# Performance work log

Measured on AMD Instinct MI355X. Metric: run time of the kernel, lower is better.

Reference implementation:

```python
import jax, jax.numpy as jnp
import numpy as np

NUM_HEADS = 16


def rotate_half(x):
    h = x.shape[-1] // 2
    return jnp.concatenate([-x[..., h:], x[..., :h]], axis=-1)


def setup_inputs() -> dict:
    key = jax.random.key(0)
    ks = jax.random.split(key, 8)
    S, dim, hd = 8192, 1280, 80
    n_seg = 8
    hidden_states = jax.random.normal(ks[0], (S, dim), dtype=jnp.float32)
    cu_seqlens = (jnp.arange(n_seg + 1, dtype=jnp.int32) * (S // n_seg))
    ang = jax.random.uniform(ks[1], (S, hd), dtype=jnp.float32) * (2.0 * np.pi)
    cos = jnp.cos(ang)
    sin = jnp.sin(ang)
    qkv_w = jax.random.normal(ks[2], (3 * dim, dim), dtype=jnp.float32) * (dim ** -0.5)
    qkv_b = jax.random.normal(ks[3], (3 * dim,), dtype=jnp.float32) * 0.02
    proj_w = jax.random.normal(ks[4], (dim, dim), dtype=jnp.float32) * (dim ** -0.5)
    proj_b = jax.random.normal(ks[5], (dim,), dtype=jnp.float32) * 0.02
    return {"hidden_states": hidden_states, "cu_seqlens": cu_seqlens,
            "cos": cos, "sin": sin, "qkv_w": qkv_w, "qkv_b": qkv_b,
            "proj_w": proj_w, "proj_b": proj_b}


def reference(hidden_states, cu_seqlens, cos, sin, qkv_w, qkv_b, proj_w, proj_b):
    S, dim = hidden_states.shape
    H = NUM_HEADS
    hd = dim // H
    scaling = hd ** -0.5

    # qkv projection: [S, 3*dim] -> [S, 3, H, hd]
    qkv = (hidden_states @ qkv_w.T + qkv_b).reshape(S, 3, H, hd)
    q, k, v = qkv[:, 0], qkv[:, 1], qkv[:, 2]  # each [S, H, hd]

    # RoPE in float32, cos/sin broadcast over heads
    c = cos[:, None, :].astype(jnp.float32)
    s = sin[:, None, :].astype(jnp.float32)
    qf, kf = q.astype(jnp.float32), k.astype(jnp.float32)
    q = (qf * c + rotate_half(qf) * s).astype(q.dtype)
    k = (kf * c + rotate_half(kf) * s).astype(k.dtype)

    # Block-diagonal varlen attention: equal-length segments -> batch dim
    lengths = np.diff(np.asarray(cu_seqlens))
    L = int(lengths[0])
    assert (lengths == L).all(), "reference assumes uniform segment lengths"
    B = lengths.shape[0]
    qb = q.reshape(B, L, H, hd)
    kb = k.reshape(B, L, H, hd)
    vb = v.reshape(B, L, H, hd)

    scores = jnp.einsum('blhd,bmhd->bhlm', qb, kb) * scaling
    probs = jax.nn.softmax(scores.astype(jnp.float32), axis=-1).astype(scores.dtype)
    out = jnp.einsum('bhlm,bmhd->blhd', probs, vb).reshape(S, dim)

    return out @ proj_w.T + proj_b
```

## Files before the change

### kernel.cpp

```cpp
#include <hip/hip_runtime.h>
#include <math.h>

typedef _Float16 f16;
typedef _Float16 half8 __attribute__((ext_vector_type(8)));
typedef _Float16 half4v __attribute__((ext_vector_type(4)));
typedef _Float16 half2v __attribute__((ext_vector_type(2)));
typedef float floatx4 __attribute__((ext_vector_type(4)));
typedef unsigned int u32;

#define AS1 __attribute__((address_space(1)))
#define AS3 __attribute__((address_space(3)))

__device__ __forceinline__ void stage16(f16* l, const f16* g) {
    __builtin_amdgcn_global_load_lds((const AS1 u32*)g, (AS3 u32*)l, 16, 0, 0);
}

__global__ __launch_bounds__(256) void cvt_f32_f16(const float* __restrict__ in,
                                                   f16* __restrict__ out, int n4) {
    int i = blockIdx.x * blockDim.x + threadIdx.x;
    if (i >= n4) return;
    float4 v = ((const float4*)in)[i];
    half4v h = {(f16)v.x, (f16)v.y, (f16)v.z, (f16)v.w};
    ((half4v*)out)[i] = h;
}

constexpr int GK = 1280;

__global__ __launch_bounds__(256) void gemm_nt(const f16* __restrict__ A,
                                               const f16* __restrict__ B,
                                               const float* __restrict__ bias,
                                               f16* __restrict__ outH,
                                               float* __restrict__ outF, int N) {
    __shared__ f16 As[128 * 32];
    __shared__ f16 Bs[128 * 32];
    const int t = threadIdx.x;
    const int lane = t & 63;
    const int w = t >> 6;
    const int wm = w & 1, wn = w >> 1;
    const int c16 = lane & 15, quad = lane >> 4;
    const size_t bm = blockIdx.x, bn = blockIdx.y;
    const f16* Ab = A + bm * 128 * GK;
    const f16* Bb = B + bn * 128 * GK;
    floatx4 acc[4][4] = {};
    const int c0 = t, c1 = t + 256;
    for (int k0 = 0; k0 < GK; k0 += 32) {
        stage16(As + c0 * 8, Ab + (size_t)(c0 >> 2) * GK + k0 + (c0 & 3) * 8);
        stage16(As + c1 * 8, Ab + (size_t)(c1 >> 2) * GK + k0 + (c1 & 3) * 8);
        stage16(Bs + c0 * 8, Bb + (size_t)(c0 >> 2) * GK + k0 + (c0 & 3) * 8);
        stage16(Bs + c1 * 8, Bb + (size_t)(c1 >> 2) * GK + k0 + (c1 & 3) * 8);
        __syncthreads();
        half8 af[4], bf[4];
#pragma unroll
        for (int i = 0; i < 4; i++)
            af[i] = *(const half8*)(As + (wm * 64 + i * 16 + c16) * 32 + quad * 8);
#pragma unroll
        for (int j = 0; j < 4; j++)
            bf[j] = *(const half8*)(Bs + (wn * 64 + j * 16 + c16) * 32 + quad * 8);
#pragma unroll
        for (int i = 0; i < 4; i++)
#pragma unroll
            for (int j = 0; j < 4; j++)
                acc[i][j] = __builtin_amdgcn_mfma_f32_16x16x32_f16(af[i], bf[j], acc[i][j], 0, 0, 0);
        __syncthreads();
    }
#pragma unroll
    for (int i = 0; i < 4; i++) {
#pragma unroll
        for (int j = 0; j < 4; j++) {
            const int col = (int)bn * 128 + wn * 64 + j * 16 + c16;
            const float bv = bias[col];
#pragma unroll
            for (int r = 0; r < 4; r++) {
                const size_t row = bm * 128 + wm * 64 + i * 16 + quad * 4 + r;
                const float v = acc[i][j][r] + bv;
                if (outH) outH[row * (size_t)N + col] = (f16)v;
                else      outF[row * (size_t)N + col] = v;
            }
        }
    }
}

#define QSCALE (0.11180339887498949f * 1.4426950408889634f)

__global__ __launch_bounds__(256) void rope_kernel(const f16* __restrict__ qkv,
                                                   const float* __restrict__ cosp,
                                                   const float* __restrict__ sinp,
                                                   f16* __restrict__ qb, f16* __restrict__ kb,
                                                   f16* __restrict__ vt) {
    constexpr int S = 8192;
    const int bs = blockIdx.x, h = blockIdx.y, t = threadIdx.x;
    for (int j = t; j < 64 * 40; j += 256) {
        int sl = j / 40, d = j % 40;
        int s = bs * 64 + sl;
        float c0 = cosp[s * 80 + d], c1 = cosp[s * 80 + d + 40];
        float n0 = sinp[s * 80 + d], n1 = sinp[s * 80 + d + 40];
        size_t base = (size_t)s * 3840 + h * 80;
        float q0 = (float)qkv[base + d], q1 = (float)qkv[base + d + 40];
        float k0 = (float)qkv[base + 1280 + d], k1 = (float)qkv[base + 1280 + d + 40];
        size_t ob = ((size_t)h * S + s) * 96;
        qb[ob + d]      = (f16)((q0 * c0 - q1 * n0) * QSCALE);
        qb[ob + d + 40] = (f16)((q1 * c1 + q0 * n1) * QSCALE);
        kb[ob + d]      = (f16)(k0 * c0 - k1 * n0);
        kb[ob + d + 40] = (f16)(k1 * c1 + k0 * n1);
    }
    for (int j = t; j < 64 * 16; j += 256) {
        int sl = j >> 4, dp = 80 + (j & 15);
        size_t ob = ((size_t)h * S + bs * 64 + sl) * 96;
        qb[ob + dp] = (dp == 80) ? (f16)(-8.0f) : (f16)0.f;
        kb[ob + dp] = (dp == 80) ? (f16)(1.0f) : (f16)0.f;
    }
    __shared__ f16 vls[64][81];
    for (int j = t; j < 64 * 80; j += 256) {
        int sl = j / 80, d = j % 80;
        vls[sl][d] = qkv[((size_t)(bs * 64 + sl)) * 3840 + 2560 + h * 80 + d];
    }
    __syncthreads();
    for (int j = t; j < 64 * 80; j += 256) {
        int d = j >> 6, sl = j & 63;
        vt[((size_t)(h * 80 + d)) * S + bs * 64 + sl] = vls[sl][d];
    }
}

__global__ __launch_bounds__(256, 3) void attn_kernel(const f16* __restrict__ qb,
                                                      const f16* __restrict__ kb,
                                                      const f16* __restrict__ vt,
                                                      const int* __restrict__ cu,
                                                      f16* __restrict__ out) {
    constexpr int S = 8192;
    __shared__ f16 Ks[2][64 * 96];
    __shared__ f16 Ps[128 * 72];
    const int t = threadIdx.x, lane = t & 63, w = t >> 6;
    const int c16 = lane & 15, quad = lane >> 4;
    const int qt = blockIdx.x, h = blockIdx.y, z = blockIdx.z;
    const int s0 = cu[z];

    half8 qf[2][3];
#pragma unroll
    for (int qt2 = 0; qt2 < 2; qt2++)
#pragma unroll
        for (int ks = 0; ks < 3; ks++)
            qf[qt2][ks] = *(const half8*)(qb + ((size_t)h * S + s0 + qt * 128 + w * 32 + qt2 * 16 + c16) * 96 + ks * 32 + quad * 8);

    const f16 ov = (c16 == 0) ? (f16)1.f : (f16)0.f;
    const half8 onesf = {ov, ov, ov, ov, ov, ov, ov, ov};

    {
        const f16* Kg = kb + ((size_t)h * S + s0) * 96;
#pragma unroll
        for (int i = 0; i < 3; i++) { int c = t + i * 256; stage16(&Ks[0][0] + c * 8, Kg + c * 8); }
    }
    __syncthreads();

    floatx4 o[6][2] = {};

    for (int kv = 0; kv < 16; kv++) {
        if (kv < 15) {
            const f16* Kg = kb + ((size_t)h * S + s0 + (kv + 1) * 64) * 96;
            f16* Kd = &Ks[(kv + 1) & 1][0];
#pragma unroll
            for (int i = 0; i < 3; i++) { int c = t + i * 256; stage16(Kd + c * 8, Kg + c * 8); }
        }
        const f16* Kc = &Ks[kv & 1][0];
        floatx4 sc[4][2] = {};
#pragma unroll
        for (int ks = 0; ks < 3; ks++) {
            half8 kf[4];
#pragma unroll
            for (int mt = 0; mt < 4; mt++)
                kf[mt] = *(const half8*)(Kc + (mt * 16 + c16) * 96 + ks * 32 + quad * 8);
#pragma unroll
            for (int qt2 = 0; qt2 < 2; qt2++)
#pragma unroll
                for (int mt = 0; mt < 4; mt++)
                    sc[mt][qt2] = __builtin_amdgcn_mfma_f32_16x16x32_f16(kf[mt], qf[qt2][ks], sc[mt][qt2], 0, 0, 0);
        }
#pragma unroll
        for (int qt2 = 0; qt2 < 2; qt2++) {
            const int q = w * 32 + qt2 * 16 + c16;
#pragma unroll
            for (int mt = 0; mt < 4; mt++) {
                half4v pv;
#pragma unroll
                for (int r = 0; r < 4; r++)
                    pv[r] = (f16)__builtin_amdgcn_exp2f(sc[mt][qt2][r]);
                *(half4v*)(Ps + q * 72 + mt * 16 + quad * 4) = pv;
            }
        }
#pragma unroll
        for (int ks = 0; ks < 2; ks++) {
            const f16* Vg = vt + (size_t)h * 80 * S + s0 + kv * 64 + ks * 32;
            half8 vf[5];
#pragma unroll
            for (int dt = 0; dt < 5; dt++)
                vf[dt] = *(const half8*)(Vg + (size_t)(dt * 16 + c16) * S + quad * 8);
#pragma unroll
            for (int qt2 = 0; qt2 < 2; qt2++) {
                const int q = w * 32 + qt2 * 16 + c16;
                half8 pf = *(const half8*)(Ps + q * 72 + ks * 32 + quad * 8);
#pragma unroll
                for (int dt = 0; dt < 5; dt++)
                    o[dt][qt2] = __builtin_amdgcn_mfma_f32_16x16x32_f16(vf[dt], pf, o[dt][qt2], 0, 0, 0);
                o[5][qt2] = __builtin_amdgcn_mfma_f32_16x16x32_f16(onesf, pf, o[5][qt2], 0, 0, 0);
            }
        }
        __syncthreads();
    }
#pragma unroll
    for (int qt2 = 0; qt2 < 2; qt2++) {
        const float l = __shfl(o[5][qt2][0], c16);
        const float inv = 1.f / l;
        const size_t srow = (size_t)s0 + qt * 128 + w * 32 + qt2 * 16 + c16;
#pragma unroll
        for (int dt = 0; dt < 5; dt++)
#pragma unroll
            for (int rp = 0; rp < 2; rp++) {
                half2v hv = {(f16)(o[dt][qt2][rp * 2] * inv), (f16)(o[dt][qt2][rp * 2 + 1] * inv)};
                *(half2v*)(out + srow * 1280 + h * 80 + dt * 16 + quad * 4 + rp * 2) = hv;
            }
    }
}

extern "C" void kernel_launch(void* const* d_in, const int* in_sizes, int n_in,
                              void* d_out, int out_size, void* d_ws, size_t ws_size,
                              hipStream_t stream) {
    const float* hidden = (const float*)d_in[0];
    const int* cu       = (const int*)d_in[1];
    const float* cosp   = (const float*)d_in[2];
    const float* sinp   = (const float*)d_in[3];
    const float* qkv_w  = (const float*)d_in[4];
    const float* qkv_b  = (const float*)d_in[5];
    const float* proj_w = (const float*)d_in[6];
    const float* proj_b = (const float*)d_in[7];
    float* out = (float*)d_out;

    constexpr size_t S = 8192, DIM = 1280, N3 = 3840;
    f16* A16   = (f16*)d_ws;
    f16* W16   = A16 + S * DIM;
    f16* P16   = W16 + N3 * DIM;
    f16* QKV16 = P16 + DIM * DIM;
    f16* QB    = QKV16 + S * N3;
    f16* KB    = QB + (size_t)16 * S * 96;
    f16* VT    = KB + (size_t)16 * S * 96;
    f16* AT16  = A16;

    {
        int n4 = (int)(S * DIM / 4);
        cvt_f32_f16<<<(n4 + 255) / 256, 256, 0, stream>>>(hidden, A16, n4);
    }
    {
        int n4 = (int)(N3 * DIM / 4);
        cvt_f32_f16<<<(n4 + 255) / 256, 256, 0, stream>>>(qkv_w, W16, n4);
    }
    {
        int n4 = (int)(DIM * DIM / 4);
        cvt_f32_f16<<<(n4 + 255) / 256, 256, 0, stream>>>(proj_w, P16, n4);
    }
    gemm_nt<<<dim3(64, 30), 256, 0, stream>>>(A16, W16, qkv_b, QKV16, nullptr, 3840);
    rope_kernel<<<dim3(128, 16), 256, 0, stream>>>(QKV16, cosp, sinp, QB, KB, VT);
    attn_kernel<<<dim3(8, 16, 8), 256, 0, stream>>>(QB, KB, VT, cu, AT16);
    gemm_nt<<<dim3(64, 10), 256, 0, stream>>>(AT16, P16, proj_b, nullptr, out, 1280);
}
```

Baseline: 409.3 us.

## Use k-chunk-major LDS layout in GEMM and attention; vectorize RoPE kernel

The GEMM and attention K staging now store 16-byte chunks in LDS in k-chunk-major order, so each quad's half8 reads come from contiguous rows. This is meant to remove the LDS bank conflicts caused by the row-major stride-32/96 layout. The RoPE kernel is rewritten so each thread handles eight elements with half8 loads and stores, using 320 threads per block. In exchange, global loads during staging become less contiguous per wavefront, which could reduce coalescing.

```diff
diff --git a/kernel.cpp b/kernel.cpp
--- a/kernel.cpp
+++ b/kernel.cpp
@@ -43,19 +43,21 @@
     const f16* Bb = B + bn * 128 * GK;
     floatx4 acc[4][4] = {};
     const int c0 = t, c1 = t + 256;
+    const int r0 = c0 & 127, kc0 = c0 >> 7;
+    const int r1 = c1 & 127, kc1 = c1 >> 7;
     for (int k0 = 0; k0 < GK; k0 += 32) {
-        stage16(As + c0 * 8, Ab + (size_t)(c0 >> 2) * GK + k0 + (c0 & 3) * 8);
-        stage16(As + c1 * 8, Ab + (size_t)(c1 >> 2) * GK + k0 + (c1 & 3) * 8);
-        stage16(Bs + c0 * 8, Bb + (size_t)(c0 >> 2) * GK + k0 + (c0 & 3) * 8);
-        stage16(Bs + c1 * 8, Bb + (size_t)(c1 >> 2) * GK + k0 + (c1 & 3) * 8);
+        stage16(As + c0 * 8, Ab + (size_t)r0 * GK + k0 + kc0 * 8);
+        stage16(As + c1 * 8, Ab + (size_t)r1 * GK + k0 + kc1 * 8);
+        stage16(Bs + c0 * 8, Bb + (size_t)r0 * GK + k0 + kc0 * 8);
+        stage16(Bs + c1 * 8, Bb + (size_t)r1 * GK + k0 + kc1 * 8);
         __syncthreads();
         half8 af[4], bf[4];
 #pragma unroll
         for (int i = 0; i < 4; i++)
-            af[i] = *(const half8*)(As + (wm * 64 + i * 16 + c16) * 32 + quad * 8);
+            af[i] = *(const half8*)(As + (quad * 128 + wm * 64 + i * 16 + c16) * 8);
 #pragma unroll
         for (int j = 0; j < 4; j++)
-            bf[j] = *(const half8*)(Bs + (wn * 64 + j * 16 + c16) * 32 + quad * 8);
+            bf[j] = *(const half8*)(Bs + (quad * 128 + wn * 64 + j * 16 + c16) * 8);
 #pragma unroll
         for (int i = 0; i < 4; i++)
 #pragma unroll
@@ -82,42 +84,57 @@
 
 #define QSCALE (0.11180339887498949f * 1.4426950408889634f)
 
-__global__ __launch_bounds__(256) void rope_kernel(const f16* __restrict__ qkv,
+__global__ __launch_bounds__(320) void rope_kernel(const f16* __restrict__ qkv,
                                                    const float* __restrict__ cosp,
                                                    const float* __restrict__ sinp,
                                                    f16* __restrict__ qb, f16* __restrict__ kb,
                                                    f16* __restrict__ vt) {
     constexpr int S = 8192;
     const int bs = blockIdx.x, h = blockIdx.y, t = threadIdx.x;
-    for (int j = t; j < 64 * 40; j += 256) {
-        int sl = j / 40, d = j % 40;
-        int s = bs * 64 + sl;
-        float c0 = cosp[s * 80 + d], c1 = cosp[s * 80 + d + 40];
-        float n0 = sinp[s * 80 + d], n1 = sinp[s * 80 + d + 40];
-        size_t base = (size_t)s * 3840 + h * 80;
-        float q0 = (float)qkv[base + d], q1 = (float)qkv[base + d + 40];
-        float k0 = (float)qkv[base + 1280 + d], k1 = (float)qkv[base + 1280 + d + 40];
-        size_t ob = ((size_t)h * S + s) * 96;
-        qb[ob + d]      = (f16)((q0 * c0 - q1 * n0) * QSCALE);
-        qb[ob + d + 40] = (f16)((q1 * c1 + q0 * n1) * QSCALE);
-        kb[ob + d]      = (f16)(k0 * c0 - k1 * n0);
-        kb[ob + d + 40] = (f16)(k1 * c1 + k0 * n1);
-    }
-    for (int j = t; j < 64 * 16; j += 256) {
-        int sl = j >> 4, dp = 80 + (j & 15);
-        size_t ob = ((size_t)h * S + bs * 64 + sl) * 96;
-        qb[ob + dp] = (dp == 80) ? (f16)(-8.0f) : (f16)0.f;
-        kb[ob + dp] = (dp == 80) ? (f16)(1.0f) : (f16)0.f;
+    const int sl = t / 5, g = t % 5;
+    const int s = bs * 64 + sl;
+    {
+        const size_t base = (size_t)s * 3840 + h * 80 + g * 8;
+        half8 qa = *(const half8*)(qkv + base);
+        half8 qc = *(const half8*)(qkv + base + 40);
+        half8 ka = *(const half8*)(qkv + base + 1280);
+        half8 kc = *(const half8*)(qkv + base + 1320);
+        const float* cp = cosp + (size_t)s * 80 + g * 8;
+        const float* sp = sinp + (size_t)s * 80 + g * 8;
+        half8 qo0, qo1, ko0, ko1;
+#pragma unroll
+        for (int j = 0; j < 8; j++) {
+            float c0 = cp[j], c1 = cp[j + 40];
+            float n0 = sp[j], n1 = sp[j + 40];
+            float q0 = (float)qa[j], q1 = (float)qc[j];
+            float k0 = (float)ka[j], k1 = (float)kc[j];
+            qo0[j] = (f16)((q0 * c0 - q1 * n0) * QSCALE);
+            qo1[j] = (f16)((q1 * c1 + q0 * n1) * QSCALE);
+            ko0[j] = (f16)(k0 * c0 - k1 * n0);
+            ko1[j] = (f16)(k1 * c1 + k0 * n1);
+        }
+        const size_t ob = ((size_t)h * S + s) * 96 + g * 8;
+        *(half8*)(qb + ob)      = qo0;
+        *(half8*)(qb + ob + 40) = qo1;
+        *(half8*)(kb + ob)      = ko0;
+        *(half8*)(kb + ob + 40) = ko1;
+        if (g < 2) {
+            half8 qp = {}, kp = {};
+            if (g == 0) { qp[0] = (f16)(-8.0f); kp[0] = (f16)(1.0f); }
+            const size_t pb = ((size_t)h * S + s) * 96 + 80 + g * 8;
+            *(half8*)(qb + pb) = qp;
+            *(half8*)(kb + pb) = kp;
+        }
     }
     __shared__ f16 vls[64][81];
-    for (int j = t; j < 64 * 80; j += 256) {
-        int sl = j / 80, d = j % 80;
-        vls[sl][d] = qkv[((size_t)(bs * 64 + sl)) * 3840 + 2560 + h * 80 + d];
+    for (int j = t; j < 64 * 80; j += 320) {
+        int s2 = j / 80, d = j % 80;
+        vls[s2][d] = qkv[((size_t)(bs * 64 + s2)) * 3840 + 2560 + h * 80 + d];
     }
     __syncthreads();
-    for (int j = t; j < 64 * 80; j += 256) {
-        int d = j >> 6, sl = j & 63;
-        vt[((size_t)(h * 80 + d)) * S + bs * 64 + sl] = vls[sl][d];
+    for (int j = t; j < 64 * 80; j += 320) {
+        int d = j >> 6, s2 = j & 63;
+        vt[((size_t)(h * 80 + d)) * S + bs * 64 + s2] = vls[s2][d];
     }
 }
 
@@ -144,10 +161,16 @@
     const f16 ov = (c16 == 0) ? (f16)1.f : (f16)0.f;
     const half8 onesf = {ov, ov, ov, ov, ov, ov, ov, ov};
 
+    const int sc0 = t, sc1 = t + 256, sc2 = t + 512;
+    const int sr0 = sc0 & 63, sk0 = sc0 >> 6;
+    const int sr1 = sc1 & 63, sk1 = sc1 >> 6;
+    const int sr2 = sc2 & 63, sk2 = sc2 >> 6;
+
     {
         const f16* Kg = kb + ((size_t)h * S + s0) * 96;
-#pragma unroll
-        for (int i = 0; i < 3; i++) { int c = t + i * 256; stage16(&Ks[0][0] + c * 8, Kg + c * 8); }
+        stage16(&Ks[0][0] + sc0 * 8, Kg + (size_t)sr0 * 96 + sk0 * 8);
+        stage16(&Ks[0][0] + sc1 * 8, Kg + (size_t)sr1 * 96 + sk1 * 8);
+        stage16(&Ks[0][0] + sc2 * 8, Kg + (size_t)sr2 * 96 + sk2 * 8);
     }
     __syncthreads();
 
@@ -157,8 +180,9 @@
         if (kv < 15) {
             const f16* Kg = kb + ((size_t)h * S + s0 + (kv + 1) * 64) * 96;
             f16* Kd = &Ks[(kv + 1) & 1][0];
-#pragma unroll
-            for (int i = 0; i < 3; i++) { int c = t + i * 256; stage16(Kd + c * 8, Kg + c * 8); }
+            stage16(Kd + sc0 * 8, Kg + (size_t)sr0 * 96 + sk0 * 8);
+            stage16(Kd + sc1 * 8, Kg + (size_t)sr1 * 96 + sk1 * 8);
+            stage16(Kd + sc2 * 8, Kg + (size_t)sr2 * 96 + sk2 * 8);
         }
         const f16* Kc = &Ks[kv & 1][0];
         floatx4 sc[4][2] = {};
@@ -167,7 +191,7 @@
             half8 kf[4];
 #pragma unroll
             for (int mt = 0; mt < 4; mt++)
-                kf[mt] = *(const half8*)(Kc + (mt * 16 + c16) * 96 + ks * 32 + quad * 8);
+                kf[mt] = *(const half8*)(Kc + ((ks * 4 + quad) * 64 + mt * 16 + c16) * 8);
 #pragma unroll
             for (int qt2 = 0; qt2 < 2; qt2++)
 #pragma unroll
@@ -256,7 +280,7 @@
         cvt_f32_f16<<<(n4 + 255) / 256, 256, 0, stream>>>(proj_w, P16, n4);
     }
     gemm_nt<<<dim3(64, 30), 256, 0, stream>>>(A16, W16, qkv_b, QKV16, nullptr, 3840);
-    rope_kernel<<<dim3(128, 16), 256, 0, stream>>>(QKV16, cosp, sinp, QB, KB, VT);
+    rope_kernel<<<dim3(128, 16), 320, 0, stream>>>(QKV16, cosp, sinp, QB, KB, VT);
     attn_kernel<<<dim3(8, 16, 8), 256, 0, stream>>>(QB, KB, VT, cu, AT16);
     gemm_nt<<<dim3(64, 10), 256, 0, stream>>>(AT16, P16, proj_b, nullptr, out, 1280);
 }
```

Result: slower. 508.7 us (+24.3%).
